# Kernel optimization log

Measured on AMD Instinct MI355X. Metric: run time of the kernel, lower is better.

The kernel has to match this reference:

```python
import jax, jax.numpy as jnp
import numpy as np

N = 50000          # nodes
E = 800000         # edges (avg degree 16)
IN_DIM = 64        # input feature dim
HEADS = 8          # heads in hidden layers
T = 3              # num edge types
NUM_CLASSES = 16   # output layer: 1 head, hidden = num_classes
SLOPE = 0.2        # LeakyReLU negative slope


def typed_linear(x, etype, W):
    # x: [E, din], W: [T, din, dout] -> per-edge-type linear (grouped GEMM)
    out = jnp.zeros((x.shape[0], W.shape[2]), dtype=x.dtype)
    for t in range(W.shape[0]):  # small fixed loop over edge types
        out = out + jnp.where((etype == t)[:, None], x @ W[t], jnp.zeros((), x.dtype))
    return out


def edge_softmax(scores, dst, n):
    # segmented softmax over incoming edges of each dst node; scores: [E, H]
    m = jax.ops.segment_max(scores, dst, num_segments=n)
    e = jnp.exp(scores - m[dst])
    s = jax.ops.segment_sum(e, dst, num_segments=n)
    return e / s[dst]


def hetsann_conv(x, src, dst, etype, W, a_l, a_r, heads, res, act, n):
    ne = src.shape[0]
    m = x[src]                                   # copy_u: gather src features to edges
    feat = typed_linear(m, etype, W)             # [E, heads*d]
    d = feat.shape[1] // heads
    h_l = typed_linear(feat, etype, a_l).reshape(ne, heads, d).sum(-1)  # [E, H]
    h_r = typed_linear(feat, etype, a_r).reshape(ne, heads, d).sum(-1)  # [E, H]
    att = jax.nn.leaky_relu(h_l + h_r, SLOPE)    # [E, H]
    alpha = edge_softmax(att, dst, n)            # [E, H]
    # attention-weighted messages, scatter-summed to dst (HetSANN eq. 5)
    msg = (feat.reshape(ne, heads, d) * alpha[:, :, None]).reshape(ne, heads * d)
    out = jax.ops.segment_sum(msg, dst, num_segments=n)  # [N, heads*d]
    if res is not None:
        w, b = res
        out = out + x @ w + b
    if act:
        out = jax.nn.elu(out)
    return out


def setup_inputs() -> dict:
    key = jax.random.key(0)
    ks = jax.random.split(key, 14)
    s = 1.0 / np.sqrt(IN_DIM)
    s2 = 1.0 / np.sqrt(NUM_CLASSES)
    return {
        "x": jax.random.normal(ks[0], (N, IN_DIM), dtype=jnp.float32),
        "src": jax.random.randint(ks[1], (E,), 0, N),
        "dst": jax.random.randint(ks[2], (E,), 0, N),
        "ntype": jax.random.randint(ks[3], (N,), 0, T),
        "etype": jax.random.randint(ks[4], (E,), 0, T),
        # layer 0: TypedLinear(64 -> 64), heads=8
        "W1": jax.random.normal(ks[5], (T, IN_DIM, IN_DIM), dtype=jnp.float32) * s,
        "al1": jax.random.normal(ks[6], (T, IN_DIM, IN_DIM), dtype=jnp.float32) * s,
        "ar1": jax.random.normal(ks[7], (T, IN_DIM, IN_DIM), dtype=jnp.float32) * s,
        # layer 1 (output): TypedLinear(64 -> 16), heads=1, residual Linear(64 -> 16)
        "W2": jax.random.normal(ks[8], (T, IN_DIM, NUM_CLASSES), dtype=jnp.float32) * s,
        "al2": jax.random.normal(ks[9], (T, NUM_CLASSES, NUM_CLASSES), dtype=jnp.float32) * s2,
        "ar2": jax.random.normal(ks[10], (T, NUM_CLASSES, NUM_CLASSES), dtype=jnp.float32) * s2,
        "res_w": jax.random.normal(ks[11], (IN_DIM, NUM_CLASSES), dtype=jnp.float32) * s,
        "res_b": jax.random.normal(ks[12], (NUM_CLASSES,), dtype=jnp.float32) * 0.01,
    }


def reference(x, src, dst, ntype, etype, W1, al1, ar1, W2, al2, ar2, res_w, res_b):
    # layer 0: 8 heads, no residual, ELU activation (dropout=0 -> identity)
    h = hetsann_conv(x, src, dst, etype, W1, al1, ar1, HEADS, None, True, N)
    # output layer: 1 head, hidden=num_classes, residual, no activation
    h = hetsann_conv(h, src, dst, etype, W2, al2, ar2, 1, (res_w, res_b), False, N)
    # dgl.mean_nodes over the single graph
    return h.mean(axis=0)  # [NUM_CLASSES]
```

## Files before the change

kernel.cpp:

```cpp
#include <hip/hip_runtime.h>
#include <hip/hip_bf16.h>

typedef unsigned int u32;
typedef unsigned short u16;

#define NN 50000
#define EE 800000
#define TT 3

#define OFF_C1     0
#define OFF_C2     1536
#define OFF_CNT    1728
#define OFF_FLAG   51728
#define OFF_OPART  51732
#define OFF_ROWPTR 52756
#define OFF_CNT2   102760
#define OFF_CW1    102760
#define OFF_CW2    117096
#define OFF_BSUM   152760
#define OFF_PSRC   153016
#define OFF_PK1    953024
#define OFF_PK2    953024
#define OFF_H      5753024

__device__ __forceinline__ float bf2f(u32 u) {
    union { u32 i; float f; } v; v.i = u << 16; return v.f;
}
__device__ __forceinline__ u32 f2bf(float f) {
    union { float f; u32 i; } v; v.f = f;
    return (v.i + 0x7fffu + ((v.i >> 16) & 1u)) >> 16;
}

__global__ void precompute(const float* __restrict__ W1, const float* __restrict__ al1,
                           const float* __restrict__ ar1, const float* __restrict__ W2,
                           const float* __restrict__ al2, const float* __restrict__ ar2,
                           float* __restrict__ ws) {
    __shared__ float a1c[64][8];
    __shared__ float a2c[16];
    int t = blockIdx.x;
    int tid = threadIdx.x;
    {
        int k2 = tid >> 3, hh = tid & 7;
        float s = 0.f;
#pragma unroll
        for (int j = 0; j < 8; ++j) {
            int idx = t * 4096 + k2 * 64 + hh * 8 + j;
            s += al1[idx] + ar1[idx];
        }
        a1c[k2][hh] = s;
    }
    if (tid < 16) {
        float s = 0.f;
#pragma unroll
        for (int j = 0; j < 16; ++j) {
            int idx = t * 256 + tid * 16 + j;
            s += al2[idx] + ar2[idx];
        }
        a2c[tid] = s;
    }
    __syncthreads();
    {
        int k = tid >> 3, hh = tid & 7;
        float s = 0.f;
#pragma unroll
        for (int k2 = 0; k2 < 64; ++k2)
            s += W1[t * 4096 + k * 64 + k2] * a1c[k2][hh];
        ws[OFF_C1 + t * 512 + k * 8 + hh] = s;
    }
    if (tid < 64) {
        float s = 0.f;
#pragma unroll
        for (int k2 = 0; k2 < 16; ++k2)
            s += W2[t * 1024 + tid * 16 + k2] * a2c[k2];
        ws[OFF_C2 + t * 64 + tid] = s;
    }
}

__global__ __launch_bounds__(256) void hist_k(const int* __restrict__ dst, int* wsi) {
    int e = blockIdx.x * 256 + threadIdx.x;
    if (e < EE) atomicAdd(wsi + OFF_CNT + dst[e], 1);
}

__global__ __launch_bounds__(256) void scan1(int* wsi) {
    __shared__ int sd[256];
    int t = threadIdx.x;
    int i = blockIdx.x * 256 + t;
    int v = (i < NN) ? wsi[OFF_CNT + i] : 0;
    sd[t] = v;
    __syncthreads();
    for (int o = 128; o > 0; o >>= 1) {
        if (t < o) sd[t] += sd[t + o];
        __syncthreads();
    }
    if (t == 0) wsi[OFF_BSUM + blockIdx.x] = sd[0];
}

__global__ __launch_bounds__(256) void scan2(int* wsi) {
    __shared__ int sd[256];
    int t = threadIdx.x;
    int v = (t < 196) ? wsi[OFF_BSUM + t] : 0;
    sd[t] = v;
    __syncthreads();
    for (int o = 1; o < 256; o <<= 1) {
        int u = (t >= o) ? sd[t - o] : 0;
        __syncthreads();
        sd[t] += u;
        __syncthreads();
    }
    wsi[OFF_BSUM + t] = sd[t] - v;
    if (t == 0) wsi[OFF_ROWPTR + NN] = EE;
}

__global__ __launch_bounds__(256) void scan3(int* wsi) {
    __shared__ int sd[256];
    int t = threadIdx.x;
    int i = blockIdx.x * 256 + t;
    int v = (i < NN) ? wsi[OFF_CNT + i] : 0;
    sd[t] = v;
    __syncthreads();
    for (int o = 1; o < 256; o <<= 1) {
        int u = (t >= o) ? sd[t - o] : 0;
        __syncthreads();
        sd[t] += u;
        __syncthreads();
    }
    if (i < NN) {
        int ex = wsi[OFF_BSUM + blockIdx.x] + sd[t] - v;
        wsi[OFF_ROWPTR + i] = ex;
        wsi[OFF_CNT2 + i] = ex;
    }
}

__global__ __launch_bounds__(256) void scatter_k(const int* __restrict__ src, const int* __restrict__ dst,
                          const int* __restrict__ etype, int* wsi) {
    int e = blockIdx.x * 256 + threadIdx.x;
    if (e >= EE) return;
    int d = dst[e];
    int slot = atomicAdd(wsi + OFF_CNT2 + d, 1);
    wsi[OFF_PSRC + slot] = src[e] | (etype[e] << 20);
}

__global__ __launch_bounds__(256) void fill_cw(const float* __restrict__ W1, const float* __restrict__ W2,
                        const float* __restrict__ res_w, float* __restrict__ ws) {
    int idx = blockIdx.x * 256 + threadIdx.x;
    if (idx < 14336) {
        int k = idx / 224, c = idx - k * 224;
        float v;
        if (c < 192) v = W1[(c >> 6) * 4096 + k * 64 + (c & 63)];
        else if (c < 216) v = ws[OFF_C1 + ((c - 192) >> 3) * 512 + k * 8 + ((c - 192) & 7)];
        else v = 0.f;
        ws[OFF_CW1 + idx] = v;
    }
    if (idx < 4352) {
        int k = idx / 68, c = idx - k * 68;
        float v;
        if (c < 48) v = W2[(c >> 4) * 1024 + k * 16 + (c & 15)];
        else if (c < 51) v = ws[OFF_C2 + (c - 48) * 64 + k];
        else if (c < 67) v = res_w[k * 16 + (c - 51)];
        else v = 0.f;
        ws[OFF_CW2 + idx] = v;
    }
}

__global__ __launch_bounds__(512) void gemm_f(const float* __restrict__ x, const float* __restrict__ cw,
                       float* __restrict__ ws) {
    __shared__ alignas(16) float Xs[64 * 65];
    int tid = threadIdx.x;
    int wave = __builtin_amdgcn_readfirstlane(tid >> 6);
    int lane = tid & 63;
    int n0 = blockIdx.x * 64;
    {
        const float4* xg = (const float4*)(x + (size_t)n0 * 64);
        for (int q = tid; q < 1024; q += 512) {
            int row = q >> 4;
            float4 v = (n0 + row < NN) ? xg[q] : make_float4(0.f, 0.f, 0.f, 0.f);
            *(float4*)(Xs + row * 65 + (q & 15) * 4) = v;
        }
    }
    __syncthreads();
    int cbase = wave * 28;
    float acc[28];
#pragma unroll
    for (int i = 0; i < 28; ++i) acc[i] = 0.f;
    const float* xrow = Xs + lane * 65;
    float wA[28], wB[28];
#pragma unroll
    for (int j = 0; j < 28; ++j) wA[j] = cw[cbase + j];
    for (int k = 0; k < 64; k += 2) {
#pragma unroll
        for (int j = 0; j < 28; ++j) wB[j] = cw[(k + 1) * 224 + cbase + j];
        float xv = xrow[k];
#pragma unroll
        for (int j = 0; j < 28; ++j) acc[j] = fmaf(xv, wA[j], acc[j]);
        if (k + 2 < 64) {
#pragma unroll
            for (int j = 0; j < 28; ++j) wA[j] = cw[(k + 2) * 224 + cbase + j];
        }
        float xv2 = xrow[k + 1];
#pragma unroll
        for (int j = 0; j < 28; ++j) acc[j] = fmaf(xv2, wB[j], acc[j]);
    }
    int n = n0 + lane;
    if (n < NN) {
        u32* row = (u32*)ws + OFF_PK1 + (size_t)n * 96;
#pragma unroll
        for (int g = 0; g < 7; ++g) {
            int col = cbase + 4 * g;
            float v0 = acc[4*g], v1 = acc[4*g+1], v2 = acc[4*g+2], v3 = acc[4*g+3];
            if (col < 192) {
                int t = col >> 6, ci = col & 63;
                int dw = __builtin_amdgcn_cvt_pk_fp8_f32(v0, v1, 0, false);
                dw = __builtin_amdgcn_cvt_pk_fp8_f32(v2, v3, dw, true);
                row[t * 32 + (ci >> 2)] = (u32)dw;
            } else if (col < 216) {
                int jj = col - 192;
                int t = jj >> 3, rem = jj & 7;
                v0 = v0 > 0.f ? v0 : 0.2f * v0;
                v1 = v1 > 0.f ? v1 : 0.2f * v1;
                v2 = v2 > 0.f ? v2 : 0.2f * v2;
                v3 = v3 > 0.f ? v3 : 0.2f * v3;
                row[t * 32 + 16 + (rem >> 1)]     = f2bf(__expf(v0)) | (f2bf(__expf(v1)) << 16);
                row[t * 32 + 16 + (rem >> 1) + 1] = f2bf(__expf(v2)) | (f2bf(__expf(v3)) << 16);
            }
        }
    }
}

__global__ __launch_bounds__(256) void agg1(const int* __restrict__ wsi, float* __restrict__ ws) {
    int tid = threadIdx.x;
    int wave = tid >> 6, lane = tid & 63;
    int q = lane >> 4;
    int cg = lane & 15;
    int d = blockIdx.x * 4 + wave;
    int epw = cg >> 2;
    int sh_ep = ((cg >> 1) & 1) * 16;
    int start = wsi[OFF_ROWPTR + d], end = wsi[OFF_ROWPTR + d + 1];
    const u32* pk = (const u32*)ws + OFF_PK1;
    const int* psrc = wsi + OFF_PSRC;
    float acc0 = 0.f, acc1 = 0.f, acc2 = 0.f, acc3 = 0.f, den = 0.f;
    int s = start + q;
    u32 fdw_c = 0, epdw_c = 0;
    int p1 = 0;
    bool valid = s < end;
    if (valid) {
        int p = psrc[s];
        int sn = p & 0xFFFFF, t = p >> 20;
        size_t base = (size_t)(sn * 3 + t) * 32;
        fdw_c = pk[base + cg];
        epdw_c = pk[base + 16 + epw];
    }
    if (s + 4 < end) p1 = psrc[s + 4];
    while (valid) {
        u32 fdw = fdw_c, epdw = epdw_c;
        bool v1 = s + 4 < end;
        if (v1) {
            int sn = p1 & 0xFFFFF, t = p1 >> 20;
            size_t base = (size_t)(sn * 3 + t) * 32;
            fdw_c = pk[base + cg];
            epdw_c = pk[base + 16 + epw];
        }
        if (s + 8 < end) p1 = psrc[s + 8];
        float w = bf2f((epdw >> sh_ep) & 0xffffu);
        float m0 = __builtin_amdgcn_cvt_f32_fp8((int)fdw, 0);
        float m1 = __builtin_amdgcn_cvt_f32_fp8((int)(fdw >> 8), 0);
        float m2 = __builtin_amdgcn_cvt_f32_fp8((int)(fdw >> 16), 0);
        float m3 = __builtin_amdgcn_cvt_f32_fp8((int)(fdw >> 24), 0);
        den += w;
        acc0 += w * m0;
        acc1 += w * m1;
        acc2 += w * m2;
        acc3 += w * m3;
        s += 4;
        valid = v1;
    }
    acc0 += __shfl_xor(acc0, 16); acc0 += __shfl_xor(acc0, 32);
    acc1 += __shfl_xor(acc1, 16); acc1 += __shfl_xor(acc1, 32);
    acc2 += __shfl_xor(acc2, 16); acc2 += __shfl_xor(acc2, 32);
    acc3 += __shfl_xor(acc3, 16); acc3 += __shfl_xor(acc3, 32);
    den  += __shfl_xor(den, 16);  den  += __shfl_xor(den, 32);
    if (q == 0) {
        float dn = (end > start) ? den : 1.f;
        float v0 = acc0 / dn, v1 = acc1 / dn, v2 = acc2 / dn, v3 = acc3 / dn;
        v0 = v0 > 0.f ? v0 : __expf(v0) - 1.f;
        v1 = v1 > 0.f ? v1 : __expf(v1) - 1.f;
        v2 = v2 > 0.f ? v2 : __expf(v2) - 1.f;
        v3 = v3 > 0.f ? v3 : __expf(v3) - 1.f;
        *(float4*)(ws + OFF_H + (size_t)d * 64 + cg * 4) = make_float4(v0, v1, v2, v3);
    }
}

__global__ __launch_bounds__(256) void gemm_f2(const float* __restrict__ cw, float* __restrict__ ws) {
    __shared__ alignas(16) float Hs[64 * 65];
    __shared__ float Rs[64][17];
    int tid = threadIdx.x;
    int wave = __builtin_amdgcn_readfirstlane(tid >> 6);
    int lane = tid & 63;
    int n0 = blockIdx.x * 64;
    {
        const float4* hg = (const float4*)(ws + OFF_H + (size_t)n0 * 64);
        for (int q = tid; q < 1024; q += 256) {
            int row = q >> 4;
            float4 v = (n0 + row < NN) ? hg[q] : make_float4(0.f, 0.f, 0.f, 0.f);
            *(float4*)(Hs + row * 65 + (q & 15) * 4) = v;
        }
    }
    __syncthreads();
    int cbase = wave * 17;
    float acc[17];
#pragma unroll
    for (int i = 0; i < 17; ++i) acc[i] = 0.f;
    const float* hrow = Hs + lane * 65;
    float wA[17], wB[17];
#pragma unroll
    for (int j = 0; j < 17; ++j) wA[j] = cw[cbase + j];
    for (int k = 0; k < 64; k += 2) {
#pragma unroll
        for (int j = 0; j < 17; ++j) wB[j] = cw[(k + 1) * 68 + cbase + j];
        float hv = hrow[k];
#pragma unroll
        for (int j = 0; j < 17; ++j) acc[j] = fmaf(hv, wA[j], acc[j]);
        if (k + 2 < 64) {
#pragma unroll
            for (int j = 0; j < 17; ++j) wA[j] = cw[(k + 2) * 68 + cbase + j];
        }
        float hv2 = hrow[k + 1];
#pragma unroll
        for (int j = 0; j < 17; ++j) acc[j] = fmaf(hv2, wB[j], acc[j]);
    }
    int n = n0 + lane;
    u16* pk2u = (u16*)((u32*)ws + OFF_PK2);
#pragma unroll
    for (int i = 0; i < 17; ++i) {
        int col = cbase + i;
        if (col < 48) {
            if (n < NN) {
                int t = col >> 4, c2 = col & 15;
                pk2u[((size_t)n * 3 + t) * 32 + c2] = (u16)f2bf(acc[i]);
            }
        } else if (col < 51) {
            if (n < NN) {
                float v = acc[i]; v = v > 0.f ? v : 0.2f * v;
                ws[OFF_PK2 + ((size_t)n * 3 + (col - 48)) * 16 + 8] = __expf(v);
            }
        } else if (col < 67) {
            Rs[lane][col - 51] = acc[i];
        }
    }
    __syncthreads();
    if (tid < 16) {
        float s = 0.f;
#pragma unroll 8
        for (int r = 0; r < 64; ++r) s += Rs[r][tid];
        atomicAdd(ws + OFF_OPART + (blockIdx.x & 63) * 16 + tid, s);
    }
}

__global__ __launch_bounds__(256) void agg2(const int* __restrict__ wsi, float* __restrict__ ws) {
    __shared__ float outs[4][16];
    int tid = threadIdx.x;
    int wave = tid >> 6, lane = tid & 63;
    int q = lane >> 4, c = lane & 15;
    int d = blockIdx.x * 4 + wave;
    int start = wsi[OFF_ROWPTR + d], end = wsi[OFF_ROWPTR + d + 1];
    const u16* pk2u = (const u16*)((const u32*)ws + OFF_PK2);
    const float* pk2f = ws + OFF_PK2;
    const int* psrc = wsi + OFF_PSRC;
    float acc = 0.f, den = 0.f;
    int s = start + q;
    float w_c = 0.f, m_c = 0.f;
    bool valid = s < end;
    if (valid) {
        int p = psrc[s];
        int sn = p & 0xFFFFF, t = p >> 20;
        size_t r = (size_t)(sn * 3 + t);
        w_c = pk2f[r * 16 + 8];
        m_c = bf2f(pk2u[r * 32 + c]);
    }
    while (valid) {
        float w = w_c, m = m_c;
        int s2 = s + 4;
        bool v2 = s2 < end;
        if (v2) {
            int p = psrc[s2];
            int sn = p & 0xFFFFF, t = p >> 20;
            size_t r = (size_t)(sn * 3 + t);
            w_c = pk2f[r * 16 + 8];
            m_c = bf2f(pk2u[r * 32 + c]);
        }
        den += w;
        acc += w * m;
        s = s2; valid = v2;
    }
    acc += __shfl_xor(acc, 16);
    acc += __shfl_xor(acc, 32);
    den += __shfl_xor(den, 16);
    den += __shfl_xor(den, 32);
    float val = (end > start) ? acc / den : 0.f;
    if (q == 0) outs[wave][c] = val;
    __syncthreads();
    if (tid < 16) {
        float sum = outs[0][tid] + outs[1][tid] + outs[2][tid] + outs[3][tid];
        atomicAdd(ws + OFF_OPART + (blockIdx.x & 63) * 16 + tid, sum);
    }
}

__global__ void final_k(const float* __restrict__ res_b, float* __restrict__ ws, float* __restrict__ out) {
    int c = threadIdx.x;
    if (c < 16) {
        float s = 0.f;
        for (int r = 0; r < 64; ++r) s += ws[OFF_OPART + r * 16 + c];
        out[c] = s * (1.0f / (float)NN) + res_b[c];
    }
}

extern "C" void kernel_launch(void* const* d_in, const int* in_sizes, int n_in,
                              void* d_out, int out_size, void* d_ws, size_t ws_size,
                              hipStream_t stream) {
    const float* x     = (const float*)d_in[0];
    const int*   src   = (const int*)d_in[1];
    const int*   dst   = (const int*)d_in[2];
    const int*   etype = (const int*)d_in[4];
    const float* W1    = (const float*)d_in[5];
    const float* al1   = (const float*)d_in[6];
    const float* ar1   = (const float*)d_in[7];
    const float* W2    = (const float*)d_in[8];
    const float* al2   = (const float*)d_in[9];
    const float* ar2   = (const float*)d_in[10];
    const float* res_w = (const float*)d_in[11];
    const float* res_b = (const float*)d_in[12];
    float* ws = (float*)d_ws;
    int* wsi = (int*)d_ws;
    float* out = (float*)d_out;

    hipMemsetAsync((char*)d_ws + (size_t)OFF_CNT * 4, 0, (size_t)51028 * 4, stream);
    hipLaunchKernelGGL(precompute, dim3(TT), dim3(512), 0, stream, W1, al1, ar1, W2, al2, ar2, ws);
    hipLaunchKernelGGL(hist_k, dim3((EE + 255) / 256), dim3(256), 0, stream, dst, wsi);
    hipLaunchKernelGGL(scan1, dim3(196), dim3(256), 0, stream, wsi);
    hipLaunchKernelGGL(scan2, dim3(1), dim3(256), 0, stream, wsi);
    hipLaunchKernelGGL(scan3, dim3(196), dim3(256), 0, stream, wsi);
    hipLaunchKernelGGL(scatter_k, dim3((EE + 255) / 256), dim3(256), 0, stream, src, dst, etype, wsi);
    hipLaunchKernelGGL(fill_cw, dim3(56), dim3(256), 0, stream, W1, W2, res_w, ws);
    hipLaunchKernelGGL(gemm_f, dim3((NN + 63) / 64), dim3(512), 0, stream, x, ws + OFF_CW1, ws);
    hipLaunchKernelGGL(agg1, dim3(NN / 4), dim3(256), 0, stream, wsi, ws);
    hipLaunchKernelGGL(gemm_f2, dim3((NN + 63) / 64), dim3(256), 0, stream, ws + OFF_CW2, ws);
    hipLaunchKernelGGL(agg2, dim3(NN / 4), dim3(256), 0, stream, wsi, ws);
    hipLaunchKernelGGL(final_k, dim3(1), dim3(64), 0, stream, res_b, ws, out);
}
```

Measured before the change: 316.3 us.

## Replace atomic histogram CSR build with two-pass bucketed counting sort

Replaces the global per-node histogram, three-kernel scan and per-edge global-atomic scatter with a two-level bucketed sort. The first pass bins edges by destination high bits using shared-memory histograms and one global atomic per bucket per block. The second pass sorts each bucket locally by the low destination bits to produce row pointers and packed source/type entries. This cuts global atomics and launch count, but assumes each bucket fits in an 8192-entry stride and packs the source index into 16 bits, while N is 50000.

```diff
diff --git a/kernel.cpp b/kernel.cpp
--- a/kernel.cpp
+++ b/kernel.cpp
@@ -3,23 +3,26 @@
 
 typedef unsigned int u32;
 typedef unsigned short u16;
+typedef unsigned char u8;
 
 #define NN 50000
 #define EE 800000
 #define TT 3
+#define NBUCK 196
+#define BSTRIDE 8192
+#define P1_CHUNK 4096
 
 #define OFF_C1     0
 #define OFF_C2     1536
-#define OFF_CNT    1728
-#define OFF_FLAG   51728
-#define OFF_OPART  51732
+#define OFF_BCNT   1728
+#define OFF_OPART  1984
+#define OFF_BBASE  3008
 #define OFF_ROWPTR 52756
-#define OFF_CNT2   102760
 #define OFF_CW1    102760
 #define OFF_CW2    117096
-#define OFF_BSUM   152760
 #define OFF_PSRC   153016
 #define OFF_PK1    953024
+#define OFF_TMP    953024
 #define OFF_PK2    953024
 #define OFF_H      5753024
 
@@ -74,70 +77,6 @@
             s += W2[t * 1024 + tid * 16 + k2] * a2c[k2];
         ws[OFF_C2 + t * 64 + tid] = s;
     }
-}
-
-__global__ __launch_bounds__(256) void hist_k(const int* __restrict__ dst, int* wsi) {
-    int e = blockIdx.x * 256 + threadIdx.x;
-    if (e < EE) atomicAdd(wsi + OFF_CNT + dst[e], 1);
-}
-
-__global__ __launch_bounds__(256) void scan1(int* wsi) {
-    __shared__ int sd[256];
-    int t = threadIdx.x;
-    int i = blockIdx.x * 256 + t;
-    int v = (i < NN) ? wsi[OFF_CNT + i] : 0;
-    sd[t] = v;
-    __syncthreads();
-    for (int o = 128; o > 0; o >>= 1) {
-        if (t < o) sd[t] += sd[t + o];
-        __syncthreads();
-    }
-    if (t == 0) wsi[OFF_BSUM + blockIdx.x] = sd[0];
-}
-
-__global__ __launch_bounds__(256) void scan2(int* wsi) {
-    __shared__ int sd[256];
-    int t = threadIdx.x;
-    int v = (t < 196) ? wsi[OFF_BSUM + t] : 0;
-    sd[t] = v;
-    __syncthreads();
-    for (int o = 1; o < 256; o <<= 1) {
-        int u = (t >= o) ? sd[t - o] : 0;
-        __syncthreads();
-        sd[t] += u;
-        __syncthreads();
-    }
-    wsi[OFF_BSUM + t] = sd[t] - v;
-    if (t == 0) wsi[OFF_ROWPTR + NN] = EE;
-}
-
-__global__ __launch_bounds__(256) void scan3(int* wsi) {
-    __shared__ int sd[256];
-    int t = threadIdx.x;
-    int i = blockIdx.x * 256 + t;
-    int v = (i < NN) ? wsi[OFF_CNT + i] : 0;
-    sd[t] = v;
-    __syncthreads();
-    for (int o = 1; o < 256; o <<= 1) {
-        int u = (t >= o) ? sd[t - o] : 0;
-        __syncthreads();
-        sd[t] += u;
-        __syncthreads();
-    }
-    if (i < NN) {
-        int ex = wsi[OFF_BSUM + blockIdx.x] + sd[t] - v;
-        wsi[OFF_ROWPTR + i] = ex;
-        wsi[OFF_CNT2 + i] = ex;
-    }
-}
-
-__global__ __launch_bounds__(256) void scatter_k(const int* __restrict__ src, const int* __restrict__ dst,
-                          const int* __restrict__ etype, int* wsi) {
-    int e = blockIdx.x * 256 + threadIdx.x;
-    if (e >= EE) return;
-    int d = dst[e];
-    int slot = atomicAdd(wsi + OFF_CNT2 + d, 1);
-    wsi[OFF_PSRC + slot] = src[e] | (etype[e] << 20);
 }
 
 __global__ __launch_bounds__(256) void fill_cw(const float* __restrict__ W1, const float* __restrict__ W2,
@@ -159,6 +98,91 @@
         else if (c < 67) v = res_w[k * 16 + (c - 51)];
         else v = 0.f;
         ws[OFF_CW2 + idx] = v;
+    }
+}
+
+__global__ __launch_bounds__(256) void sort_p1(const int* __restrict__ src, const int* __restrict__ dst,
+                        const int* __restrict__ etype, int* wsi) {
+    __shared__ u32 Est[P1_CHUNK];
+    __shared__ u8 Bst[P1_CHUNK];
+    __shared__ int hist[NBUCK], base[NBUCK];
+    int tid = threadIdx.x;
+    int e0 = blockIdx.x * P1_CHUNK;
+    int cnt = EE - e0; if (cnt > P1_CHUNK) cnt = P1_CHUNK;
+    for (int i = tid; i < NBUCK; i += 256) hist[i] = 0;
+    __syncthreads();
+    for (int i = tid; i < cnt; i += 256) {
+        int e = e0 + i;
+        int s = src[e], d = dst[e], t = etype[e];
+        int b = d >> 8;
+        Est[i] = (u32)s | ((u32)t << 16) | ((u32)(d & 255) << 18);
+        Bst[i] = (u8)b;
+        atomicAdd(&hist[b], 1);
+    }
+    __syncthreads();
+    for (int i = tid; i < NBUCK; i += 256) {
+        int h = hist[i];
+        base[i] = h ? atomicAdd(wsi + OFF_BCNT + i, h) : 0;
+        hist[i] = 0;
+    }
+    __syncthreads();
+    for (int i = tid; i < cnt; i += 256) {
+        int b = Bst[i];
+        int idx = base[b] + atomicAdd(&hist[b], 1);
+        wsi[OFF_TMP + b * BSTRIDE + idx] = (int)Est[i];
+    }
+}
+
+__global__ __launch_bounds__(256) void sort_p2a(int* wsi) {
+    __shared__ int sd[256];
+    int t = threadIdx.x;
+    int v = (t < NBUCK) ? wsi[OFF_BCNT + t] : 0;
+    sd[t] = v;
+    __syncthreads();
+    for (int o = 1; o < 256; o <<= 1) {
+        int u = (t >= o) ? sd[t - o] : 0;
+        __syncthreads();
+        sd[t] += u;
+        __syncthreads();
+    }
+    if (t < NBUCK) wsi[OFF_BBASE + t] = sd[t] - v;
+    if (t == 0) wsi[OFF_ROWPTR + NN] = EE;
+}
+
+__global__ __launch_bounds__(256) void sort_p2(int* wsi) {
+    __shared__ int cnt[256], sd[256], lrpx[256];
+    int b = blockIdx.x;
+    int tid = threadIdx.x;
+    int nb = wsi[OFF_BCNT + b];
+    int gbase = wsi[OFF_BBASE + b];
+    cnt[tid] = 0;
+    __syncthreads();
+    const int* tmp = wsi + OFF_TMP + b * BSTRIDE;
+    for (int i = tid; i < nb; i += 256) {
+        int e = tmp[i];
+        atomicAdd(&cnt[(e >> 18) & 255], 1);
+    }
+    __syncthreads();
+    int v = cnt[tid];
+    sd[tid] = v;
+    __syncthreads();
+    for (int o = 1; o < 256; o <<= 1) {
+        int u = (tid >= o) ? sd[tid - o] : 0;
+        __syncthreads();
+        sd[tid] += u;
+        __syncthreads();
+    }
+    int ex = sd[tid] - v;
+    lrpx[tid] = ex;
+    int d = b * 256 + tid;
+    if (d < NN) wsi[OFF_ROWPTR + d] = gbase + ex;
+    cnt[tid] = 0;
+    __syncthreads();
+    for (int i = tid; i < nb; i += 256) {
+        int e = tmp[i];
+        int dres = (e >> 18) & 255;
+        int slot = gbase + lrpx[dres] + atomicAdd(&cnt[dres], 1);
+        wsi[OFF_PSRC + slot] = (e & 0xFFFF) | (((e >> 16) & 3) << 20);
     }
 }
 
@@ -432,14 +456,12 @@
     int* wsi = (int*)d_ws;
     float* out = (float*)d_out;
 
-    hipMemsetAsync((char*)d_ws + (size_t)OFF_CNT * 4, 0, (size_t)51028 * 4, stream);
+    hipMemsetAsync((char*)d_ws + (size_t)OFF_BCNT * 4, 0, (size_t)1280 * 4, stream);
     hipLaunchKernelGGL(precompute, dim3(TT), dim3(512), 0, stream, W1, al1, ar1, W2, al2, ar2, ws);
-    hipLaunchKernelGGL(hist_k, dim3((EE + 255) / 256), dim3(256), 0, stream, dst, wsi);
-    hipLaunchKernelGGL(scan1, dim3(196), dim3(256), 0, stream, wsi);
-    hipLaunchKernelGGL(scan2, dim3(1), dim3(256), 0, stream, wsi);
-    hipLaunchKernelGGL(scan3, dim3(196), dim3(256), 0, stream, wsi);
-    hipLaunchKernelGGL(scatter_k, dim3((EE + 255) / 256), dim3(256), 0, stream, src, dst, etype, wsi);
     hipLaunchKernelGGL(fill_cw, dim3(56), dim3(256), 0, stream, W1, W2, res_w, ws);
+    hipLaunchKernelGGL(sort_p1, dim3((EE + P1_CHUNK - 1) / P1_CHUNK), dim3(256), 0, stream, src, dst, etype, wsi);
+    hipLaunchKernelGGL(sort_p2a, dim3(1), dim3(256), 0, stream, wsi);
+    hipLaunchKernelGGL(sort_p2, dim3(NBUCK), dim3(256), 0, stream, wsi);
     hipLaunchKernelGGL(gemm_f, dim3((NN + 63) / 64), dim3(512), 0, stream, x, ws + OFF_CW1, ws);
     hipLaunchKernelGGL(agg1, dim3(NN / 4), dim3(256), 0, stream, wsi, ws);
     hipLaunchKernelGGL(gemm_f2, dim3((NN + 63) / 64), dim3(256), 0, stream, ws + OFF_CW2, ws);
```

Result: faster. 253.9 us (-19.7%).
